# Kernel optimization log

Hardware: AMD Instinct MI355X
Metric: run time of the kernel (lower is better)

## Reference

```python
import jax, jax.numpy as jnp
import numpy as np

H = 4  # num_heads
LN_EPS = 1e-5


def setup_inputs() -> dict:
    key = jax.random.key(0)
    ks = jax.random.split(key, 6)
    B, N, IN, OUT = 4, 2048, 256, 256
    return {
        "node_feats": jax.random.normal(ks[0], (B, N, IN), dtype=jnp.float32),
        "adj_matrix": jax.random.uniform(ks[1], (B, N, N), dtype=jnp.float32),
        "W_lin": jax.random.normal(ks[2], (IN, OUT), dtype=jnp.float32) * (IN ** -0.5),
        "b_lin": jnp.zeros((OUT,), dtype=jnp.float32),
        "W_q": jax.random.normal(ks[3], (IN, OUT), dtype=jnp.float32) * (IN ** -0.5),
        "W_k": jax.random.normal(ks[4], (IN, OUT), dtype=jnp.float32) * (IN ** -0.5),
        "ln_g": jnp.ones((OUT,), dtype=jnp.float32),
        "ln_b": jnp.zeros((OUT,), dtype=jnp.float32),
    }


def _heads(x, B, N):
    # [B,N,OUT] -> [B,H,N,hd]
    return x.reshape(B, N, H, -1).transpose(0, 2, 1, 3)


def reference(node_feats, adj_matrix, W_lin, b_lin, W_q, W_k, ln_g, ln_b):
    B, N, _ = node_feats.shape
    out_dim = W_lin.shape[1]
    hd = out_dim // H
    scale = hd ** -0.5
    lrelu = lambda z: jax.nn.leaky_relu(z, 0.01)

    X = _heads(lrelu(node_feats @ W_lin + b_lin), B, N)   # [B,H,N,hd]
    q = _heads(lrelu(node_feats @ W_q), B, N)
    k = _heads(lrelu(node_feats @ W_k), B, N)

    att = jax.nn.sigmoid(jnp.einsum('bhxd,bhyd->bhxy', q, k) * scale)
    adj_h = adj_matrix[:, None] * att                     # [B,H,N,N]

    # symmetric degree normalization: D^-1/2 A D^-1/2 (broadcast form of diag_embed matmuls)
    deg = jnp.sum(adj_h, axis=-1)                         # [B,H,N]
    dis = jnp.where(deg > 0, deg ** -0.5, 0.0)
    A = dis[..., :, None] * adj_h * dis[..., None, :]

    Y = jnp.einsum('bhxy,bhyd->bhxd', A, X)
    Y = Y.transpose(0, 2, 1, 3).reshape(B, N, out_dim)

    mu = jnp.mean(Y, axis=-1, keepdims=True)
    var = jnp.mean((Y - mu) ** 2, axis=-1, keepdims=True)
    return (Y - mu) * jax.lax.rsqrt(var + LN_EPS) * ln_g + ln_b
```

## Files before the change

kernel.cpp:

```cpp
#include <hip/hip_runtime.h>
#include <hip/hip_bf16.h>

#define B_   4
#define N_   2048
#define IN_  256
#define OUT_ 256
#define H_   4
#define HD_  64
#define LN_EPS 1e-5f

typedef __bf16 bf16x8 __attribute__((ext_vector_type(8)));
typedef float  f32x4  __attribute__((ext_vector_type(4)));
typedef unsigned short u16x8 __attribute__((ext_vector_type(8)));

__device__ __forceinline__ unsigned short f2bf(float x) {
    unsigned int u = __float_as_uint(x);
    return (unsigned short)((u + 0x7FFFu + ((u >> 16) & 1u)) >> 16);
}

__global__ __launch_bounds__(256) void gemm3_kernel(
    const float* __restrict__ nf, const float* __restrict__ Wl,
    const float* __restrict__ bl, const float* __restrict__ Wq,
    const float* __restrict__ Wk,
    unsigned short* __restrict__ qb, unsigned short* __restrict__ kb,
    unsigned short* __restrict__ Xt)
{
    const int z  = blockIdx.z;
    const float* W = (z == 0) ? Wl : (z == 1 ? Wq : Wk);
    const int m0 = blockIdx.x * 64;
    const int n0 = blockIdx.y * 64;
    const int tid  = threadIdx.x;
    const int wave = tid >> 6;
    const int lane = tid & 63;
    const int lq = lane >> 4, lr = lane & 15;

    __shared__ unsigned short As[64][40];
    __shared__ unsigned short Bt[64][40];

    f32x4 acc[4] = {};

    for (int k0 = 0; k0 < IN_; k0 += 32) {
        {
            int r = tid >> 2, c = (tid & 3) * 8;
            const float* src = nf + (size_t)(m0 + r) * IN_ + k0 + c;
            u16x8 v;
            #pragma unroll
            for (int j = 0; j < 8; j++) v[j] = f2bf(src[j]);
            *(u16x8*)&As[r][c] = v;
        }
        {
            int kk = tid >> 3, c0 = (tid & 7) * 8;
            const float* src = W + (size_t)(k0 + kk) * OUT_ + n0 + c0;
            #pragma unroll
            for (int j = 0; j < 8; j++) Bt[c0 + j][kk] = f2bf(src[j]);
        }
        __syncthreads();

        bf16x8 af = *(const bf16x8*)&As[wave * 16 + lr][lq * 8];
        #pragma unroll
        for (int f = 0; f < 4; f++) {
            bf16x8 bfr = *(const bf16x8*)&Bt[f * 16 + lr][lq * 8];
            acc[f] = __builtin_amdgcn_mfma_f32_16x16x32_bf16(af, bfr, acc[f], 0, 0, 0);
        }
        __syncthreads();
    }

    #pragma unroll
    for (int f = 0; f < 4; f++) {
        int c = n0 + f * 16 + lr;
        float bias = (z == 0) ? bl[c] : 0.0f;
        #pragma unroll
        for (int r = 0; r < 4; r++) {
            int m = m0 + wave * 16 + lq * 4 + r;
            float v = acc[f][r] + bias;
            v = (v >= 0.f) ? v : 0.01f * v;
            unsigned short bv = f2bf(v);
            if (z == 0) {
                int n = m & (N_ - 1);
                int h = c >> 6, d = c & 63;
                Xt[(((size_t)(m >> 11) * H_ + h) * HD_ + d) * N_ + n] = bv;
            } else {
                unsigned short* dst = (z == 1) ? qb : kb;
                dst[(size_t)m * OUT_ + c] = bv;
            }
        }
    }
}

__global__ __launch_bounds__(256) void deg_kernel(
    const float* __restrict__ adj,
    const unsigned short* __restrict__ qb,
    const unsigned short* __restrict__ kb,
    float* __restrict__ dis)
{
    const int b  = blockIdx.y;
    const int x0 = blockIdx.x * 16;
    const int h    = threadIdx.x >> 6;
    const int lane = threadIdx.x & 63;
    const int lq = lane >> 4, lr = lane & 15;
    const float sc = -0.125f * 1.44269504088896f;

    bf16x8 qf[2];
    #pragma unroll
    for (int ks = 0; ks < 2; ks++)
        qf[ks] = *(const bf16x8*)&qb[(size_t)(b * N_ + x0 + lr) * OUT_ + h * HD_ + ks * 32 + lq * 8];

    float degp[4] = {0.f, 0.f, 0.f, 0.f};

    for (int yt = 0; yt < N_ / 64; yt++) {
        const int y0 = yt * 64;
        f32x4 S[4] = {};
        #pragma unroll
        for (int yb = 0; yb < 4; yb++) {
            #pragma unroll
            for (int ks = 0; ks < 2; ks++) {
                bf16x8 kf = *(const bf16x8*)&kb[(size_t)(b * N_ + y0 + yb * 16 + lr) * OUT_ + h * HD_ + ks * 32 + lq * 8];
                S[yb] = __builtin_amdgcn_mfma_f32_16x16x32_bf16(qf[ks], kf, S[yb], 0, 0, 0);
            }
        }
        #pragma unroll
        for (int yb = 0; yb < 4; yb++) {
            #pragma unroll
            for (int r = 0; r < 4; r++) {
                int x = x0 + lq * 4 + r;
                int y = y0 + yb * 16 + lr;
                float a = adj[((size_t)b * N_ + x) * N_ + y];
                float att = __builtin_amdgcn_rcpf(1.f + exp2f(S[yb][r] * sc));
                degp[r] += a * att;
            }
        }
    }
    #pragma unroll
    for (int r = 0; r < 4; r++) {
        float v = degp[r];
        v += __shfl_xor(v, 1); v += __shfl_xor(v, 2);
        v += __shfl_xor(v, 4); v += __shfl_xor(v, 8);
        degp[r] = v;
    }
    if (lr == 0) {
        #pragma unroll
        for (int r = 0; r < 4; r++) {
            int x = x0 + lq * 4 + r;
            float d = degp[r];
            dis[((size_t)b * H_ + h) * N_ + x] = (d > 0.f) ? rsqrtf(d) : 0.f;
        }
    }
}

__global__ __launch_bounds__(256) void out_kernel(
    const float* __restrict__ adj,
    const unsigned short* __restrict__ qb,
    const unsigned short* __restrict__ kb,
    const unsigned short* __restrict__ Xt,
    const float* __restrict__ dis,
    const float* __restrict__ ln_g,
    const float* __restrict__ ln_b,
    float* __restrict__ out)
{
    const int b  = blockIdx.y;
    const int x0 = blockIdx.x * 16;
    const int h    = threadIdx.x >> 6;
    const int lane = threadIdx.x & 63;
    const int lq = lane >> 4, lr = lane & 15;
    const float sc = -0.125f * 1.44269504088896f;

    __shared__ unsigned short wls[4][16][72];
    __shared__ float lnred[2][4][16];

    bf16x8 qf[2];
    #pragma unroll
    for (int ks = 0; ks < 2; ks++)
        qf[ks] = *(const bf16x8*)&qb[(size_t)(b * N_ + x0 + lr) * OUT_ + h * HD_ + ks * 32 + lq * 8];

    float dx[4];
    #pragma unroll
    for (int r = 0; r < 4; r++)
        dx[r] = dis[((size_t)b * H_ + h) * N_ + x0 + lq * 4 + r];

    f32x4 Y[4] = {};

    for (int yt = 0; yt < N_ / 64; yt++) {
        const int y0 = yt * 64;
        f32x4 S[4] = {};
        #pragma unroll
        for (int yb = 0; yb < 4; yb++) {
            #pragma unroll
            for (int ks = 0; ks < 2; ks++) {
                bf16x8 kf = *(const bf16x8*)&kb[(size_t)(b * N_ + y0 + yb * 16 + lr) * OUT_ + h * HD_ + ks * 32 + lq * 8];
                S[yb] = __builtin_amdgcn_mfma_f32_16x16x32_bf16(qf[ks], kf, S[yb], 0, 0, 0);
            }
        }
        #pragma unroll
        for (int yb = 0; yb < 4; yb++) {
            float dy = dis[((size_t)b * H_ + h) * N_ + y0 + yb * 16 + lr];
            #pragma unroll
            for (int r = 0; r < 4; r++) {
                int x = x0 + lq * 4 + r;
                int y = y0 + yb * 16 + lr;
                float a = adj[((size_t)b * N_ + x) * N_ + y];
                float att = __builtin_amdgcn_rcpf(1.f + exp2f(S[yb][r] * sc));
                wls[h][lq * 4 + r][yb * 16 + lr] = f2bf(a * att * dy);
            }
        }
        #pragma unroll
        for (int ks = 0; ks < 2; ks++) {
            bf16x8 wf = *(const bf16x8*)&wls[h][lr][ks * 32 + lq * 8];
            #pragma unroll
            for (int db = 0; db < 4; db++) {
                bf16x8 xf = *(const bf16x8*)&Xt[(((size_t)b * H_ + h) * HD_ + db * 16 + lr) * N_ + y0 + ks * 32 + lq * 8];
                Y[db] = __builtin_amdgcn_mfma_f32_16x16x32_bf16(wf, xf, Y[db], 0, 0, 0);
            }
        }
    }

    float s1[4] = {}, s2[4] = {};
    #pragma unroll
    for (int r = 0; r < 4; r++) {
        #pragma unroll
        for (int db = 0; db < 4; db++) {
            float v = Y[db][r] * dx[r];
            s1[r] += v; s2[r] += v * v;
        }
    }
    #pragma unroll
    for (int r = 0; r < 4; r++) {
        float a = s1[r], q2 = s2[r];
        a += __shfl_xor(a, 1); a += __shfl_xor(a, 2); a += __shfl_xor(a, 4); a += __shfl_xor(a, 8);
        q2 += __shfl_xor(q2, 1); q2 += __shfl_xor(q2, 2); q2 += __shfl_xor(q2, 4); q2 += __shfl_xor(q2, 8);
        s1[r] = a; s2[r] = q2;
    }
    if (lr == 0) {
        #pragma unroll
        for (int r = 0; r < 4; r++) {
            lnred[0][h][lq * 4 + r] = s1[r];
            lnred[1][h][lq * 4 + r] = s2[r];
        }
    }
    __syncthreads();

    float gg[4], bb[4];
    #pragma unroll
    for (int db = 0; db < 4; db++) {
        int c = h * HD_ + db * 16 + lr;
        gg[db] = ln_g[c]; bb[db] = ln_b[c];
    }
    #pragma unroll
    for (int r = 0; r < 4; r++) {
        int xr = lq * 4 + r;
        float t1 = lnred[0][0][xr] + lnred[0][1][xr] + lnred[0][2][xr] + lnred[0][3][xr];
        float t2 = lnred[1][0][xr] + lnred[1][1][xr] + lnred[1][2][xr] + lnred[1][3][xr];
        float mu  = t1 * (1.f / 256.f);
        float var = t2 * (1.f / 256.f) - mu * mu;
        float rs  = rsqrtf(var + LN_EPS);
        #pragma unroll
        for (int db = 0; db < 4; db++) {
            int c = h * HD_ + db * 16 + lr;
            float v = (Y[db][r] * dx[r] - mu) * rs * gg[db] + bb[db];
            out[((size_t)(b * N_ + x0 + xr)) * OUT_ + c] = v;
        }
    }
}

extern "C" void kernel_launch(void* const* d_in, const int* in_sizes, int n_in,
                              void* d_out, int out_size, void* d_ws, size_t ws_size,
                              hipStream_t stream) {
    const float* nf  = (const float*)d_in[0];
    const float* adj = (const float*)d_in[1];
    const float* Wl  = (const float*)d_in[2];
    const float* bl  = (const float*)d_in[3];
    const float* Wq  = (const float*)d_in[4];
    const float* Wk  = (const float*)d_in[5];
    const float* lng = (const float*)d_in[6];
    const float* lnb = (const float*)d_in[7];
    float* out = (float*)d_out;

    unsigned short* qb = (unsigned short*)d_ws;
    unsigned short* kb = qb + (size_t)B_ * N_ * OUT_;
    unsigned short* Xt = kb + (size_t)B_ * N_ * OUT_;
    float*         dis = (float*)(Xt + (size_t)B_ * N_ * OUT_);

    gemm3_kernel<<<dim3(128, 4, 3), 256, 0, stream>>>(nf, Wl, bl, Wq, Wk, qb, kb, Xt);
    deg_kernel<<<dim3(N_ / 16, B_), 256, 0, stream>>>(adj, qb, kb, dis);
    out_kernel<<<dim3(N_ / 16, B_), 256, 0, stream>>>(adj, qb, kb, Xt, dis, lng, lnb, out);
}
```

Measured before the change: 320.7 us.

## Split N-reduction across blocks, precast inputs, stage adj in LDS, fold dis into X

Adds a conversion kernel that casts node features and transposes the weights to bf16 once, so the projection GEMM reads bf16 directly without LDS staging. The degree and output passes now split the y dimension across extra grid blocks: degrees are combined with atomics and outputs go to partial buffers, which a new LayerNorm kernel sums. Adjacency tiles are loaded into shared memory with coalesced vector loads instead of strided scalar loads. The column-side D^-1/2 is folded into a pre-scaled copy of X, and bf16 packing uses a pack-convert instruction. The cost is more kernel launches, atomics, and extra global traffic for the fp32 partial outputs.

```diff
diff --git a/kernel.cpp b/kernel.cpp
--- a/kernel.cpp
+++ b/kernel.cpp
@@ -8,61 +8,70 @@
 #define H_   4
 #define HD_  64
 #define LN_EPS 1e-5f
+#define YCD_ 4
+#define YCO_ 2
 
 typedef __bf16 bf16x8 __attribute__((ext_vector_type(8)));
 typedef float  f32x4  __attribute__((ext_vector_type(4)));
 typedef unsigned short u16x8 __attribute__((ext_vector_type(8)));
+typedef unsigned int   u32x4 __attribute__((ext_vector_type(4)));
 
 __device__ __forceinline__ unsigned short f2bf(float x) {
     unsigned int u = __float_as_uint(x);
     return (unsigned short)((u + 0x7FFFu + ((u >> 16) & 1u)) >> 16);
 }
+__device__ __forceinline__ float bf2f(unsigned short u) {
+    return __uint_as_float((unsigned int)u << 16);
+}
+__device__ __forceinline__ unsigned int cvtpk(float lo, float hi) {
+    unsigned int r;
+    asm("v_cvt_pk_bf16_f32 %0, %1, %2" : "=v"(r) : "v"(lo), "v"(hi));
+    return r;
+}
+
+__global__ __launch_bounds__(256) void conv_kernel(
+    const float* __restrict__ nf, const float* __restrict__ Wl,
+    const float* __restrict__ Wq, const float* __restrict__ Wk,
+    unsigned short* __restrict__ nfb, unsigned short* __restrict__ Wt)
+{
+    const int bid = blockIdx.x, tid = threadIdx.x;
+    if (bid < 1024) {
+        size_t i = ((size_t)bid * 256 + tid) * 8;
+        u16x8 o;
+        #pragma unroll
+        for (int j = 0; j < 8; j++) o[j] = f2bf(nf[i + j]);
+        *(u16x8*)&nfb[i] = o;
+    } else {
+        int t = (bid - 1024) * 256 + tid;
+        int z = t >> 16;
+        int l = t & 65535;
+        int k = l & 255, n = l >> 8;
+        const float* W = (z == 0) ? Wl : (z == 1 ? Wq : Wk);
+        Wt[(size_t)z * 65536 + n * 256 + k] = f2bf(W[k * 256 + n]);
+    }
+}
 
 __global__ __launch_bounds__(256) void gemm3_kernel(
-    const float* __restrict__ nf, const float* __restrict__ Wl,
-    const float* __restrict__ bl, const float* __restrict__ Wq,
-    const float* __restrict__ Wk,
+    const unsigned short* __restrict__ nfb, const unsigned short* __restrict__ Wt3,
+    const float* __restrict__ bl,
     unsigned short* __restrict__ qb, unsigned short* __restrict__ kb,
     unsigned short* __restrict__ Xt)
 {
     const int z  = blockIdx.z;
-    const float* W = (z == 0) ? Wl : (z == 1 ? Wq : Wk);
-    const int m0 = blockIdx.x * 64;
-    const int n0 = blockIdx.y * 64;
-    const int tid  = threadIdx.x;
-    const int wave = tid >> 6;
-    const int lane = tid & 63;
+    const int m0 = blockIdx.x * 64, n0 = blockIdx.y * 64;
+    const int tid = threadIdx.x, wave = tid >> 6, lane = tid & 63;
     const int lq = lane >> 4, lr = lane & 15;
-
-    __shared__ unsigned short As[64][40];
-    __shared__ unsigned short Bt[64][40];
+    const unsigned short* Wt = Wt3 + (size_t)z * 65536;
 
     f32x4 acc[4] = {};
-
+    #pragma unroll 4
     for (int k0 = 0; k0 < IN_; k0 += 32) {
-        {
-            int r = tid >> 2, c = (tid & 3) * 8;
-            const float* src = nf + (size_t)(m0 + r) * IN_ + k0 + c;
-            u16x8 v;
-            #pragma unroll
-            for (int j = 0; j < 8; j++) v[j] = f2bf(src[j]);
-            *(u16x8*)&As[r][c] = v;
-        }
-        {
-            int kk = tid >> 3, c0 = (tid & 7) * 8;
-            const float* src = W + (size_t)(k0 + kk) * OUT_ + n0 + c0;
-            #pragma unroll
-            for (int j = 0; j < 8; j++) Bt[c0 + j][kk] = f2bf(src[j]);
-        }
-        __syncthreads();
-
-        bf16x8 af = *(const bf16x8*)&As[wave * 16 + lr][lq * 8];
+        bf16x8 af = *(const bf16x8*)&nfb[(size_t)(m0 + wave * 16 + lr) * IN_ + k0 + lq * 8];
         #pragma unroll
         for (int f = 0; f < 4; f++) {
-            bf16x8 bfr = *(const bf16x8*)&Bt[f * 16 + lr][lq * 8];
+            bf16x8 bfr = *(const bf16x8*)&Wt[(size_t)(n0 + f * 16 + lr) * IN_ + k0 + lq * 8];
             acc[f] = __builtin_amdgcn_mfma_f32_16x16x32_bf16(af, bfr, acc[f], 0, 0, 0);
         }
-        __syncthreads();
     }
 
     #pragma unroll
@@ -91,24 +100,27 @@
     const float* __restrict__ adj,
     const unsigned short* __restrict__ qb,
     const unsigned short* __restrict__ kb,
-    float* __restrict__ dis)
-{
-    const int b  = blockIdx.y;
-    const int x0 = blockIdx.x * 16;
-    const int h    = threadIdx.x >> 6;
-    const int lane = threadIdx.x & 63;
+    float* __restrict__ deg)
+{
+    const int b = blockIdx.y, x0 = blockIdx.x * 16, yc = blockIdx.z;
+    const int tid = threadIdx.x, h = tid >> 6, lane = tid & 63;
     const int lq = lane >> 4, lr = lane & 15;
     const float sc = -0.125f * 1.44269504088896f;
+    __shared__ __align__(16) float ads[16][68];
 
     bf16x8 qf[2];
     #pragma unroll
     for (int ks = 0; ks < 2; ks++)
         qf[ks] = *(const bf16x8*)&qb[(size_t)(b * N_ + x0 + lr) * OUT_ + h * HD_ + ks * 32 + lq * 8];
 
-    float degp[4] = {0.f, 0.f, 0.f, 0.f};
-
-    for (int yt = 0; yt < N_ / 64; yt++) {
-        const int y0 = yt * 64;
+    float degp[4] = {};
+
+    for (int yt = 0; yt < N_ / YCD_ / 64; yt++) {
+        const int y0 = yc * (N_ / YCD_) + yt * 64;
+        {
+            int r = tid >> 4, c = (tid & 15) * 4;
+            *(f32x4*)&ads[r][c] = *(const f32x4*)&adj[((size_t)b * N_ + x0 + r) * N_ + y0 + c];
+        }
         f32x4 S[4] = {};
         #pragma unroll
         for (int yb = 0; yb < 4; yb++) {
@@ -118,17 +130,17 @@
                 S[yb] = __builtin_amdgcn_mfma_f32_16x16x32_bf16(qf[ks], kf, S[yb], 0, 0, 0);
             }
         }
+        __syncthreads();
         #pragma unroll
         for (int yb = 0; yb < 4; yb++) {
             #pragma unroll
             for (int r = 0; r < 4; r++) {
-                int x = x0 + lq * 4 + r;
-                int y = y0 + yb * 16 + lr;
-                float a = adj[((size_t)b * N_ + x) * N_ + y];
+                float a = ads[lq * 4 + r][yb * 16 + lr];
                 float att = __builtin_amdgcn_rcpf(1.f + exp2f(S[yb][r] * sc));
                 degp[r] += a * att;
             }
         }
+        __syncthreads();
     }
     #pragma unroll
     for (int r = 0; r < 4; r++) {
@@ -139,48 +151,69 @@
     }
     if (lr == 0) {
         #pragma unroll
-        for (int r = 0; r < 4; r++) {
-            int x = x0 + lq * 4 + r;
-            float d = degp[r];
-            dis[((size_t)b * H_ + h) * N_ + x] = (d > 0.f) ? rsqrtf(d) : 0.f;
-        }
-    }
-}
-
-__global__ __launch_bounds__(256) void out_kernel(
+        for (int r = 0; r < 4; r++)
+            atomicAdd(&deg[((size_t)b * H_ + h) * N_ + x0 + lq * 4 + r], degp[r]);
+    }
+}
+
+__global__ __launch_bounds__(256) void scale_kernel(
+    const unsigned short* __restrict__ Xt, const float* __restrict__ deg,
+    unsigned short* __restrict__ Xs, float* __restrict__ dis)
+{
+    const int t = blockIdx.x * 256 + threadIdx.x;
+    const size_t idx = (size_t)t * 8;
+    const int bh = t >> 14;
+    const int y  = (int)(idx & (N_ - 1));
+    f32x4 g0 = *(const f32x4*)&deg[bh * N_ + y];
+    f32x4 g1 = *(const f32x4*)&deg[bh * N_ + y + 4];
+    float dv[8];
+    #pragma unroll
+    for (int j = 0; j < 4; j++) {
+        dv[j]     = (g0[j] > 0.f) ? rsqrtf(g0[j]) : 0.f;
+        dv[4 + j] = (g1[j] > 0.f) ? rsqrtf(g1[j]) : 0.f;
+    }
+    if ((t & 16383) < 256) {
+        f32x4 o0 = {dv[0], dv[1], dv[2], dv[3]};
+        f32x4 o1 = {dv[4], dv[5], dv[6], dv[7]};
+        *(f32x4*)&dis[bh * N_ + y]     = o0;
+        *(f32x4*)&dis[bh * N_ + y + 4] = o1;
+    }
+    u16x8 x = *(const u16x8*)&Xt[idx];
+    u32x4 o;
+    o[0] = cvtpk(bf2f(x[0]) * dv[0], bf2f(x[1]) * dv[1]);
+    o[1] = cvtpk(bf2f(x[2]) * dv[2], bf2f(x[3]) * dv[3]);
+    o[2] = cvtpk(bf2f(x[4]) * dv[4], bf2f(x[5]) * dv[5]);
+    o[3] = cvtpk(bf2f(x[6]) * dv[6], bf2f(x[7]) * dv[7]);
+    *(u32x4*)&Xs[idx] = o;
+}
+
+__global__ __launch_bounds__(256) void out1_kernel(
     const float* __restrict__ adj,
     const unsigned short* __restrict__ qb,
     const unsigned short* __restrict__ kb,
-    const unsigned short* __restrict__ Xt,
-    const float* __restrict__ dis,
-    const float* __restrict__ ln_g,
-    const float* __restrict__ ln_b,
-    float* __restrict__ out)
-{
-    const int b  = blockIdx.y;
-    const int x0 = blockIdx.x * 16;
-    const int h    = threadIdx.x >> 6;
-    const int lane = threadIdx.x & 63;
+    const unsigned short* __restrict__ Xs,
+    float* __restrict__ Ypart)
+{
+    const int b = blockIdx.y, x0 = blockIdx.x * 16, yc = blockIdx.z;
+    const int tid = threadIdx.x, h = tid >> 6, lane = tid & 63;
     const int lq = lane >> 4, lr = lane & 15;
     const float sc = -0.125f * 1.44269504088896f;
-
-    __shared__ unsigned short wls[4][16][72];
-    __shared__ float lnred[2][4][16];
+    __shared__ __align__(16) float ads[16][68];
+    __shared__ __align__(16) float wt[4][16][68];
 
     bf16x8 qf[2];
     #pragma unroll
     for (int ks = 0; ks < 2; ks++)
         qf[ks] = *(const bf16x8*)&qb[(size_t)(b * N_ + x0 + lr) * OUT_ + h * HD_ + ks * 32 + lq * 8];
 
-    float dx[4];
-    #pragma unroll
-    for (int r = 0; r < 4; r++)
-        dx[r] = dis[((size_t)b * H_ + h) * N_ + x0 + lq * 4 + r];
-
     f32x4 Y[4] = {};
 
-    for (int yt = 0; yt < N_ / 64; yt++) {
-        const int y0 = yt * 64;
+    for (int yt = 0; yt < N_ / YCO_ / 64; yt++) {
+        const int y0 = yc * (N_ / YCO_) + yt * 64;
+        {
+            int r = tid >> 4, c = (tid & 15) * 4;
+            *(f32x4*)&ads[r][c] = *(const f32x4*)&adj[((size_t)b * N_ + x0 + r) * N_ + y0 + c];
+        }
         f32x4 S[4] = {};
         #pragma unroll
         for (int yb = 0; yb < 4; yb++) {
@@ -190,75 +223,68 @@
                 S[yb] = __builtin_amdgcn_mfma_f32_16x16x32_bf16(qf[ks], kf, S[yb], 0, 0, 0);
             }
         }
+        __syncthreads();
         #pragma unroll
         for (int yb = 0; yb < 4; yb++) {
-            float dy = dis[((size_t)b * H_ + h) * N_ + y0 + yb * 16 + lr];
             #pragma unroll
             for (int r = 0; r < 4; r++) {
-                int x = x0 + lq * 4 + r;
-                int y = y0 + yb * 16 + lr;
-                float a = adj[((size_t)b * N_ + x) * N_ + y];
+                float a = ads[lq * 4 + r][yb * 16 + lr];
                 float att = __builtin_amdgcn_rcpf(1.f + exp2f(S[yb][r] * sc));
-                wls[h][lq * 4 + r][yb * 16 + lr] = f2bf(a * att * dy);
+                wt[h][lq * 4 + r][yb * 16 + lr] = a * att;
             }
         }
         #pragma unroll
         for (int ks = 0; ks < 2; ks++) {
-            bf16x8 wf = *(const bf16x8*)&wls[h][lr][ks * 32 + lq * 8];
+            f32x4 w0 = *(const f32x4*)&wt[h][lr][ks * 32 + lq * 8];
+            f32x4 w1 = *(const f32x4*)&wt[h][lr][ks * 32 + lq * 8 + 4];
+            union { u32x4 u; bf16x8 v; } wu;
+            wu.u[0] = cvtpk(w0[0], w0[1]);
+            wu.u[1] = cvtpk(w0[2], w0[3]);
+            wu.u[2] = cvtpk(w1[0], w1[1]);
+            wu.u[3] = cvtpk(w1[2], w1[3]);
             #pragma unroll
             for (int db = 0; db < 4; db++) {
-                bf16x8 xf = *(const bf16x8*)&Xt[(((size_t)b * H_ + h) * HD_ + db * 16 + lr) * N_ + y0 + ks * 32 + lq * 8];
-                Y[db] = __builtin_amdgcn_mfma_f32_16x16x32_bf16(wf, xf, Y[db], 0, 0, 0);
-            }
-        }
-    }
-
-    float s1[4] = {}, s2[4] = {};
-    #pragma unroll
-    for (int r = 0; r < 4; r++) {
-        #pragma unroll
-        for (int db = 0; db < 4; db++) {
-            float v = Y[db][r] * dx[r];
-            s1[r] += v; s2[r] += v * v;
-        }
-    }
-    #pragma unroll
-    for (int r = 0; r < 4; r++) {
-        float a = s1[r], q2 = s2[r];
-        a += __shfl_xor(a, 1); a += __shfl_xor(a, 2); a += __shfl_xor(a, 4); a += __shfl_xor(a, 8);
-        q2 += __shfl_xor(q2, 1); q2 += __shfl_xor(q2, 2); q2 += __shfl_xor(q2, 4); q2 += __shfl_xor(q2, 8);
-        s1[r] = a; s2[r] = q2;
-    }
-    if (lr == 0) {
-        #pragma unroll
-        for (int r = 0; r < 4; r++) {
-            lnred[0][h][lq * 4 + r] = s1[r];
-            lnred[1][h][lq * 4 + r] = s2[r];
-        }
-    }
+                bf16x8 xf = *(const bf16x8*)&Xs[(((size_t)b * H_ + h) * HD_ + db * 16 + lr) * N_ + y0 + ks * 32 + lq * 8];
+                Y[db] = __builtin_amdgcn_mfma_f32_16x16x32_bf16(wu.v, xf, Y[db], 0, 0, 0);
+            }
+        }
+        __syncthreads();
+    }
+
+    #pragma unroll
+    for (int db = 0; db < 4; db++)
+        #pragma unroll
+        for (int r = 0; r < 4; r++)
+            Ypart[((size_t)(yc * B_ + b) * N_ + x0 + lq * 4 + r) * OUT_ + h * HD_ + db * 16 + lr] = Y[db][r];
+}
+
+__global__ __launch_bounds__(256) void out2_kernel(
+    const float* __restrict__ Yp, const float* __restrict__ dis,
+    const float* __restrict__ lng, const float* __restrict__ lnb,
+    float* __restrict__ out)
+{
+    const int row = blockIdx.x;
+    const int c = threadIdx.x;
+    const size_t PS = (size_t)B_ * N_ * OUT_;
+    const size_t base = (size_t)row * OUT_ + c;
+    float v = Yp[base];
+    #pragma unroll
+    for (int p = 1; p < YCO_; p++) v += Yp[base + (size_t)p * PS];
+    const int b = row >> 11, x = row & (N_ - 1);
+    v *= dis[((size_t)b * H_ + (c >> 6)) * N_ + x];
+
+    float s1 = v, s2 = v * v;
+    #pragma unroll
+    for (int d = 1; d < 64; d <<= 1) { s1 += __shfl_xor(s1, d); s2 += __shfl_xor(s2, d); }
+    __shared__ float red[2][4];
+    if ((c & 63) == 0) { red[0][c >> 6] = s1; red[1][c >> 6] = s2; }
     __syncthreads();
-
-    float gg[4], bb[4];
-    #pragma unroll
-    for (int db = 0; db < 4; db++) {
-        int c = h * HD_ + db * 16 + lr;
-        gg[db] = ln_g[c]; bb[db] = ln_b[c];
-    }
-    #pragma unroll
-    for (int r = 0; r < 4; r++) {
-        int xr = lq * 4 + r;
-        float t1 = lnred[0][0][xr] + lnred[0][1][xr] + lnred[0][2][xr] + lnred[0][3][xr];
-        float t2 = lnred[1][0][xr] + lnred[1][1][xr] + lnred[1][2][xr] + lnred[1][3][xr];
-        float mu  = t1 * (1.f / 256.f);
-        float var = t2 * (1.f / 256.f) - mu * mu;
-        float rs  = rsqrtf(var + LN_EPS);
-        #pragma unroll
-        for (int db = 0; db < 4; db++) {
-            int c = h * HD_ + db * 16 + lr;
-            float v = (Y[db][r] * dx[r] - mu) * rs * gg[db] + bb[db];
-            out[((size_t)(b * N_ + x0 + xr)) * OUT_ + c] = v;
-        }
-    }
+    float t1 = red[0][0] + red[0][1] + red[0][2] + red[0][3];
+    float t2 = red[1][0] + red[1][1] + red[1][2] + red[1][3];
+    float mu  = t1 * (1.f / 256.f);
+    float var = t2 * (1.f / 256.f) - mu * mu;
+    float rs  = rsqrtf(var + LN_EPS);
+    out[base] = (v - mu) * rs * lng[c] + lnb[c];
 }
 
 extern "C" void kernel_launch(void* const* d_in, const int* in_sizes, int n_in,
@@ -274,12 +300,22 @@
     const float* lnb = (const float*)d_in[7];
     float* out = (float*)d_out;
 
-    unsigned short* qb = (unsigned short*)d_ws;
-    unsigned short* kb = qb + (size_t)B_ * N_ * OUT_;
-    unsigned short* Xt = kb + (size_t)B_ * N_ * OUT_;
-    float*         dis = (float*)(Xt + (size_t)B_ * N_ * OUT_);
-
-    gemm3_kernel<<<dim3(128, 4, 3), 256, 0, stream>>>(nf, Wl, bl, Wq, Wk, qb, kb, Xt);
-    deg_kernel<<<dim3(N_ / 16, B_), 256, 0, stream>>>(adj, qb, kb, dis);
-    out_kernel<<<dim3(N_ / 16, B_), 256, 0, stream>>>(adj, qb, kb, Xt, dis, lng, lnb, out);
-}
+    char* w = (char*)d_ws;
+    unsigned short* nfb = (unsigned short*)w;  w += (size_t)B_ * N_ * IN_ * 2;
+    unsigned short* Wt  = (unsigned short*)w;  w += (size_t)3 * IN_ * OUT_ * 2;
+    unsigned short* qb  = (unsigned short*)w;  w += (size_t)B_ * N_ * OUT_ * 2;
+    unsigned short* kb  = (unsigned short*)w;  w += (size_t)B_ * N_ * OUT_ * 2;
+    unsigned short* Xt  = (unsigned short*)w;  w += (size_t)B_ * N_ * OUT_ * 2;
+    unsigned short* Xs  = (unsigned short*)w;  w += (size_t)B_ * N_ * OUT_ * 2;
+    float* deg = (float*)w;                    w += (size_t)B_ * H_ * N_ * 4;
+    float* dis = (float*)w;                    w += (size_t)B_ * H_ * N_ * 4;
+    float* Yp  = (float*)w;                    w += (size_t)YCO_ * B_ * N_ * OUT_ * 4;
+
+    hipMemsetAsync(deg, 0, (size_t)B_ * H_ * N_ * 4, stream);
+    conv_kernel <<<1792, 256, 0, stream>>>(nf, Wl, Wq, Wk, nfb, Wt);
+    gemm3_kernel<<<dim3(128, 4, 3), 256, 0, stream>>>(nfb, Wt, bl, qb, kb, Xt);
+    deg_kernel  <<<dim3(N_ / 16, B_, YCD_), 256, 0, stream>>>(adj, qb, kb, deg);
+    scale_kernel<<<1024, 256, 0, stream>>>(Xt, deg, Xs, dis);
+    out1_kernel <<<dim3(N_ / 16, B_, YCO_), 256, 0, stream>>>(adj, qb, kb, Xs, Yp);
+    out2_kernel <<<B_ * N_, 256, 0, stream>>>(Yp, dis, lng, lnb, out);
+}
```

New measurement: 337.3 us. 5.2% more time.
